# Performance work log

Hardware: AMD Instinct MI355X
Metric: run time of the kernel (lower is better)

Reference implementation:

```python
import jax, jax.numpy as jnp
import numpy as np

NUM_HEADS = 16
EMBED_DIM = 1024
HEAD_DIM = EMBED_DIM // NUM_HEADS  # 64


def setup_inputs() -> dict:
    key = jax.random.key(0)
    k1, k2, k3 = jax.random.split(key, 3)
    x = jax.random.normal(k1, (2, 2048, EMBED_DIM), dtype=jnp.float32)
    # torch Linear(head_dim, 3*head_dim): weight [3*hd, hd], bias [3*hd]
    # stored here as W_qkv [hd, 3*hd] so that y = x @ W_qkv + b
    lim = 1.0 / np.sqrt(HEAD_DIM)
    W_qkv = jax.random.uniform(k2, (HEAD_DIM, 3 * HEAD_DIM), minval=-lim, maxval=lim, dtype=jnp.float32)
    b_qkv = jax.random.uniform(k3, (3 * HEAD_DIM,), minval=-lim, maxval=lim, dtype=jnp.float32)
    return {"x": x, "W_qkv": W_qkv, "b_qkv": b_qkv}


def reference(x, W_qkv, b_qkv):
    B, T, E = x.shape
    # [B, T, E] -> [B, H, T, hd]
    xh = x.reshape(B, T, NUM_HEADS, HEAD_DIM).transpose(0, 2, 1, 3)
    qkv = xh @ W_qkv + b_qkv  # [B, H, T, 3*hd], shared weights across heads
    q, k, v = jnp.split(qkv, 3, axis=-1)
    scale = 1.0 / jnp.sqrt(jnp.asarray(HEAD_DIM, dtype=x.dtype))
    scores = jnp.einsum('bhqd,bhkd->bhqk', q, k) * scale  # [B, H, T, T]
    attn = jax.nn.softmax(scores, axis=-1)
    out = jnp.einsum('bhqk,bhkd->bhqd', attn, v)  # [B, H, T, hd]
    return out.transpose(0, 2, 1, 3).reshape(B, T, E)
```

## Files before the change

### kernel.cpp

```cpp
#include <hip/hip_runtime.h>
#include <hip/hip_bf16.h>

#define T_SEQ   2048
#define EMBED   1024
#define HD      64
#define NHEADS  16
#define NBH     32
#define QSCALE  0.18033688011112042f

typedef __attribute__((ext_vector_type(8))) short short8;
typedef __attribute__((ext_vector_type(4))) float f32x4;
typedef __attribute__((ext_vector_type(2))) unsigned int uint2v;
typedef __attribute__((ext_vector_type(4))) unsigned int uint4v;

#if __has_builtin(__builtin_amdgcn_exp2f)
#define EXP2F __builtin_amdgcn_exp2f
#else
#define EXP2F exp2f
#endif

__device__ __forceinline__ ushort bf16r(float f) {
  union { float f; unsigned u; } v; v.f = f;
  return (ushort)((v.u + 0x8000u) >> 16);
}

__device__ __forceinline__ unsigned pk2bf_perm(float a, float b) {
  union { float f; unsigned u; } ua, ub; ua.f = a; ub.f = b;
  return __builtin_amdgcn_perm(ub.u + 0x8000u, ua.u + 0x8000u, 0x07060302u);
}
#if __has_builtin(__builtin_amdgcn_cvt_pk_bf16_f32)
typedef __attribute__((ext_vector_type(2))) __bf16 bf16x2;
__device__ __forceinline__ unsigned pkbf(float a, float b) {
  union { bf16x2 v; unsigned u; } c;
  c.v = __builtin_amdgcn_cvt_pk_bf16_f32(a, b);
  return c.u;
}
#else
#define pkbf pk2bf_perm
#endif

__device__ __forceinline__ uint2v pl32swap(unsigned a, unsigned b) {
#if __has_builtin(__builtin_amdgcn_permlane32_swap)
  return __builtin_amdgcn_permlane32_swap(a, b, false, false);
#else
  asm("v_permlane32_swap_b32 %0, %1" : "+v"(a), "+v"(b));
  return (uint2v){a, b};
#endif
}
__device__ __forceinline__ uint2v pl16swap(unsigned a, unsigned b) {
#if __has_builtin(__builtin_amdgcn_permlane16_swap)
  return __builtin_amdgcn_permlane16_swap(a, b, false, false);
#else
  asm("v_permlane16_swap_b32 %0, %1" : "+v"(a), "+v"(b));
  return (uint2v){a, b};
#endif
}

__device__ __forceinline__ void async16(const ushort* g, ushort* l) {
  __builtin_amdgcn_global_load_lds(
      (const __attribute__((address_space(1))) unsigned int*)g,
      (__attribute__((address_space(3))) unsigned int*)l, 16, 0, 0);
}

__global__ __launch_bounds__(256) void prep_w(const float* __restrict__ W,
                                              ushort* __restrict__ Wg) {
  const int i = blockIdx.x * 256 + threadIdx.x;
  const int d = i / 192, c = i - d * 192;
  const int phys = c * 64 + (((d >> 3) ^ (c & 7)) << 3) + (d & 7);
  Wg[phys] = bf16r(W[i]);
}

__global__ __launch_bounds__(256) void qkv_proj(
    const float* __restrict__ x, const ushort* __restrict__ Wg,
    const float* __restrict__ bias,
    ushort* __restrict__ Qws, ushort* __restrict__ Kws,
    ushort* __restrict__ Vtws) {
  __shared__ ushort WtL[192 * 64];
  __shared__ float bl[192];

  const int bx = blockIdx.x;
  const int b  = bx >> 9;
  const int h  = (bx >> 5) & 15;
  const int t0 = (bx & 31) * 64;
  const int tid = threadIdx.x;
  const int wave = tid >> 6, lane = tid & 63;
  const int quad = lane >> 4, n16 = lane & 15;

  const int trow = t0 + wave * 16 + n16;
  const float* xr = x + ((size_t)(b * T_SEQ + trow)) * EMBED + h * HD;
  short8 xa[2];
#pragma unroll
  for (int ks = 0; ks < 2; ks++) {
    f32x4 v0 = *(const f32x4*)(xr + ks * 32 + quad * 8);
    f32x4 v1 = *(const f32x4*)(xr + ks * 32 + quad * 8 + 4);
    short8 f;
    ((unsigned*)&f)[0] = pkbf(v0[0], v0[1]);
    ((unsigned*)&f)[1] = pkbf(v0[2], v0[3]);
    ((unsigned*)&f)[2] = pkbf(v1[0], v1[1]);
    ((unsigned*)&f)[3] = pkbf(v1[2], v1[3]);
    xa[ks] = f;
  }

#pragma unroll
  for (int it = 0; it < 6; it++)
    async16(Wg + it * 2048 + tid * 8, WtL + it * 2048 + wave * 512);
  if (tid < 192) bl[tid] = bias[tid];
  __syncthreads();

  const int bh = b * NHEADS + h;
  const size_t qkbase = (size_t)bh * T_SEQ * HD;
  const int tw = t0 + wave * 16;
  const int sw = n16 & 7;

#pragma unroll
  for (int nt = 0; nt < 12; nt++) {
    const ushort* wrow = WtL + (nt * 16 + n16) * 64;
    const short8 wb0 = *(short8*)(wrow + ((quad ^ sw) << 3));
    const short8 wb1 = *(short8*)(wrow + (((4 | quad) ^ sw) << 3));
    const float bv = bl[nt * 16 + n16];
    f32x4 acc = (f32x4){0.f, 0.f, 0.f, 0.f};
    acc = __builtin_amdgcn_mfma_f32_16x16x32_bf16(xa[0], wb0, acc, 0, 0, 0);
    acc = __builtin_amdgcn_mfma_f32_16x16x32_bf16(xa[1], wb1, acc, 0, 0, 0);
    if (nt < 4) {
      const int d = nt * 16 + n16;
#pragma unroll
      for (int r = 0; r < 4; r++)
        Qws[qkbase + (size_t)(tw + quad * 4 + r) * HD + d] =
            bf16r((acc[r] + bv) * QSCALE);
    } else if (nt < 8) {
      const int d = (nt - 4) * 16 + n16;
#pragma unroll
      for (int r = 0; r < 4; r++)
        Kws[qkbase + (size_t)(tw + quad * 4 + r) * HD + d] =
            bf16r(acc[r] + bv);
    } else {
      const int d = (nt - 8) * 16 + n16;
      const int tcol = tw + quad * 4;
      uint2v pk;
      pk.x = pkbf(acc[0] + bv, acc[1] + bv);
      pk.y = pkbf(acc[2] + bv, acc[3] + bv);
      *(uint2v*)(Vtws + (size_t)(bh * HD + d) * T_SEQ + tcol) = pk;
    }
  }
}

__global__ __launch_bounds__(256) void flash_attn(
    const ushort* __restrict__ Qws, const ushort* __restrict__ Kws,
    const ushort* __restrict__ Vtws, float* __restrict__ out) {
  __shared__ ushort Ks[4][64 * 64];
  __shared__ ushort Vs[4][64 * 64];

  const int bx = blockIdx.x;
  const int bh = bx & 31;
  const int q0 = (bx >> 5) * 128;
  const int b = bh >> 4, h = bh & 15;
  const int tid = threadIdx.x;
  const int wave = tid >> 6, lane = tid & 63;
  const int quad = lane >> 4, n16 = lane & 15;

  const ushort* Qb = Qws + (size_t)bh * T_SEQ * HD;
  const ushort* Kb = Kws + (size_t)bh * T_SEQ * HD;
  const ushort* Vb = Vtws + (size_t)bh * HD * T_SEQ;

  short8 qa[2][2];
#pragma unroll
  for (int hf = 0; hf < 2; hf++)
#pragma unroll
    for (int ks = 0; ks < 2; ks++) {
      const int row = q0 + wave * 32 + hf * 16 + n16;
      qa[hf][ks] = *(const short8*)(Qb + (size_t)row * HD + ks * 32 + quad * 8);
    }

  const int sr = tid >> 3, sp = tid & 7;
  const int sl = (sp ^ (sr & 7)) * 8;
  const ushort* srcK0 = Kb + (size_t)sr * HD + sl;
  const ushort* srcK1 = Kb + (size_t)(sr + 32) * HD + sl;
  const ushort* srcV0 = Vb + (size_t)sr * T_SEQ + sl;
  const ushort* srcV1 = Vb + (size_t)(sr + 32) * T_SEQ + sl;

  int foff[2];
#pragma unroll
  for (int ks = 0; ks < 2; ks++)
    foff[ks] = n16 * 64 + ((((ks << 2) | quad) ^ (n16 & 7)) << 3);

  short8 ones;
#pragma unroll
  for (int j = 0; j < 8; j++) ones[j] = (short)0x3F80;

  f32x4 o[2][4];
  f32x4 lA[2];
#pragma unroll
  for (int hf = 0; hf < 2; hf++) {
    lA[hf] = (f32x4){0.f, 0.f, 0.f, 0.f};
#pragma unroll
    for (int nt = 0; nt < 4; nt++) o[hf][nt] = (f32x4){0.f, 0.f, 0.f, 0.f};
  }

  async16(srcK0, Ks[0] + wave * 512);
  async16(srcK1, Ks[0] + 2048 + wave * 512);
  async16(srcV0, Vs[0] + wave * 512);
  async16(srcV1, Vs[0] + 2048 + wave * 512);
  async16(srcK0 + 64 * HD, Ks[1] + wave * 512);
  async16(srcK1 + 64 * HD, Ks[1] + 2048 + wave * 512);
  async16(srcV0 + 64, Vs[1] + wave * 512);
  async16(srcV1 + 64, Vs[1] + 2048 + wave * 512);

  for (int kt = 0; kt < 32; kt++) {
    const int cb = kt & 3;
    if (kt < 30) {
      const int pb = (kt + 2) & 3;
      const size_t kK = (size_t)(kt + 2) * 64 * HD;
      const size_t kV = (size_t)(kt + 2) * 64;
      async16(srcK0 + kK, Ks[pb] + wave * 512);
      async16(srcK1 + kK, Ks[pb] + 2048 + wave * 512);
      async16(srcV0 + kV, Vs[pb] + wave * 512);
      async16(srcV1 + kV, Vs[pb] + 2048 + wave * 512);
    }
    __builtin_amdgcn_sched_barrier(0);
    if (kt < 30)       asm volatile("s_waitcnt vmcnt(8)" ::: "memory");
    else if (kt == 30) asm volatile("s_waitcnt vmcnt(4)" ::: "memory");
    else               asm volatile("s_waitcnt vmcnt(0)" ::: "memory");
    __builtin_amdgcn_s_barrier();
    __builtin_amdgcn_sched_barrier(0);

    const ushort* Kt = Ks[cb];
    const ushort* Vt = Vs[cb];

    f32x4 s0[4], s1[4];
    __builtin_amdgcn_s_setprio(1);
#pragma unroll
    for (int nt = 0; nt < 4; nt++) {
      const short8 ka0 = *(short8*)(Kt + (nt << 10) + foff[0]);
      const short8 ka1 = *(short8*)(Kt + (nt << 10) + foff[1]);
      f32x4 a0 = (f32x4){0.f, 0.f, 0.f, 0.f};
      f32x4 a1 = (f32x4){0.f, 0.f, 0.f, 0.f};
      a0 = __builtin_amdgcn_mfma_f32_16x16x32_bf16(ka0, qa[0][0], a0, 0, 0, 0);
      a0 = __builtin_amdgcn_mfma_f32_16x16x32_bf16(ka1, qa[0][1], a0, 0, 0, 0);
      a1 = __builtin_amdgcn_mfma_f32_16x16x32_bf16(ka0, qa[1][0], a1, 0, 0, 0);
      a1 = __builtin_amdgcn_mfma_f32_16x16x32_bf16(ka1, qa[1][1], a1, 0, 0, 0);
      s0[nt] = a0;
      s1[nt] = a1;
    }
    __builtin_amdgcn_s_setprio(0);

    short8 pa[2][2];
#pragma unroll
    for (int hf = 0; hf < 2; hf++) {
      unsigned P01[4], P23[4];
#pragma unroll
      for (int nt = 0; nt < 4; nt++) {
        const f32x4 sv = hf ? s1[nt] : s0[nt];
        float p0 = EXP2F(sv[0]), p1 = EXP2F(sv[1]);
        float p2 = EXP2F(sv[2]), p3 = EXP2F(sv[3]);
        P01[nt] = pkbf(p0, p1);
        P23[nt] = pkbf(p2, p3);
      }
#pragma unroll
      for (int ks = 0; ks < 2; ks++) {
        uint2v tA = pl32swap(P01[2 * ks], P01[2 * ks + 1]);
        uint2v uA = pl16swap(tA.x, tA.y);
        uint2v tB = pl32swap(P23[2 * ks], P23[2 * ks + 1]);
        uint2v uB = pl16swap(tB.x, tB.y);
        union { uint4v u; short8 s; } c;
        c.u = (uint4v){uA.x, uB.x, uA.y, uB.y};
        pa[hf][ks] = c.s;
      }
    }

    __builtin_amdgcn_s_setprio(1);
#pragma unroll
    for (int nt = 0; nt < 4; nt++) {
      const short8 vb0 = *(short8*)(Vt + (nt << 10) + foff[0]);
      const short8 vb1 = *(short8*)(Vt + (nt << 10) + foff[1]);
      o[0][nt] = __builtin_amdgcn_mfma_f32_16x16x32_bf16(pa[0][0], vb0, o[0][nt], 0, 0, 0);
      o[0][nt] = __builtin_amdgcn_mfma_f32_16x16x32_bf16(pa[0][1], vb1, o[0][nt], 0, 0, 0);
      o[1][nt] = __builtin_amdgcn_mfma_f32_16x16x32_bf16(pa[1][0], vb0, o[1][nt], 0, 0, 0);
      o[1][nt] = __builtin_amdgcn_mfma_f32_16x16x32_bf16(pa[1][1], vb1, o[1][nt], 0, 0, 0);
    }
#pragma unroll
    for (int hf = 0; hf < 2; hf++) {
      lA[hf] = __builtin_amdgcn_mfma_f32_16x16x32_bf16(pa[hf][0], ones, lA[hf], 0, 0, 0);
      lA[hf] = __builtin_amdgcn_mfma_f32_16x16x32_bf16(pa[hf][1], ones, lA[hf], 0, 0, 0);
    }
    __builtin_amdgcn_s_setprio(0);
  }

#pragma unroll
  for (int hf = 0; hf < 2; hf++) {
#pragma unroll
    for (int r = 0; r < 4; r++) {
      const float rl = 1.0f / lA[hf][r];
      const int row = q0 + wave * 32 + hf * 16 + quad * 4 + r;
#pragma unroll
      for (int nt = 0; nt < 4; nt++) {
        const int d = nt * 16 + n16;
        out[(size_t)(b * T_SEQ + row) * EMBED + h * HD + d] = o[hf][nt][r] * rl;
      }
    }
  }
}

extern "C" void kernel_launch(void* const* d_in, const int* in_sizes, int n_in,
                              void* d_out, int out_size, void* d_ws, size_t ws_size,
                              hipStream_t stream) {
  (void)in_sizes; (void)n_in; (void)out_size; (void)ws_size;
  const float* x    = (const float*)d_in[0];
  const float* W    = (const float*)d_in[1];
  const float* bias = (const float*)d_in[2];
  float* out = (float*)d_out;

  const size_t elems = (size_t)NBH * T_SEQ * HD;
  ushort* Qws  = (ushort*)d_ws;
  ushort* Kws  = Qws + elems;
  ushort* Vtws = Kws + elems;
  ushort* Wg   = Vtws + elems;

  prep_w<<<dim3(48), dim3(256), 0, stream>>>(W, Wg);
  qkv_proj<<<dim3(1024), dim3(256), 0, stream>>>(x, Wg, bias, Qws, Kws, Vtws);
  flash_attn<<<dim3(512), dim3(256), 0, stream>>>(Qws, Kws, Vtws, out);
}
```

Before: 123.7 us.

## Process K/V tiles in pairs per barrier and vectorize Q/K projection stores

```diff
diff --git a/kernel.cpp b/kernel.cpp
--- a/kernel.cpp
+++ b/kernel.cpp
@@ -76,7 +76,7 @@
     ushort* __restrict__ Qws, ushort* __restrict__ Kws,
     ushort* __restrict__ Vtws) {
   __shared__ ushort WtL[192 * 64];
-  __shared__ float bl[192];
+  __shared__ __attribute__((aligned(16))) float bl[192];
 
   const int bx = blockIdx.x;
   const int b  = bx >> 9;
@@ -111,29 +111,35 @@
   const size_t qkbase = (size_t)bh * T_SEQ * HD;
   const int tw = t0 + wave * 16;
   const int sw = n16 & 7;
+  const int t = tw + n16;
 
 #pragma unroll
   for (int nt = 0; nt < 12; nt++) {
     const ushort* wrow = WtL + (nt * 16 + n16) * 64;
     const short8 wb0 = *(short8*)(wrow + ((quad ^ sw) << 3));
     const short8 wb1 = *(short8*)(wrow + (((4 | quad) ^ sw) << 3));
-    const float bv = bl[nt * 16 + n16];
-    f32x4 acc = (f32x4){0.f, 0.f, 0.f, 0.f};
-    acc = __builtin_amdgcn_mfma_f32_16x16x32_bf16(xa[0], wb0, acc, 0, 0, 0);
-    acc = __builtin_amdgcn_mfma_f32_16x16x32_bf16(xa[1], wb1, acc, 0, 0, 0);
-    if (nt < 4) {
-      const int d = nt * 16 + n16;
-#pragma unroll
-      for (int r = 0; r < 4; r++)
-        Qws[qkbase + (size_t)(tw + quad * 4 + r) * HD + d] =
-            bf16r((acc[r] + bv) * QSCALE);
-    } else if (nt < 8) {
-      const int d = (nt - 4) * 16 + n16;
-#pragma unroll
-      for (int r = 0; r < 4; r++)
-        Kws[qkbase + (size_t)(tw + quad * 4 + r) * HD + d] =
-            bf16r(acc[r] + bv);
+    if (nt < 8) {
+      f32x4 acc = (f32x4){0.f, 0.f, 0.f, 0.f};
+      acc = __builtin_amdgcn_mfma_f32_16x16x32_bf16(wb0, xa[0], acc, 0, 0, 0);
+      acc = __builtin_amdgcn_mfma_f32_16x16x32_bf16(wb1, xa[1], acc, 0, 0, 0);
+      const f32x4 bv4 = *(const f32x4*)(bl + nt * 16 + quad * 4);
+      uint2v pk;
+      if (nt < 4) {
+        const int d = nt * 16 + quad * 4;
+        pk.x = pkbf((acc[0] + bv4[0]) * QSCALE, (acc[1] + bv4[1]) * QSCALE);
+        pk.y = pkbf((acc[2] + bv4[2]) * QSCALE, (acc[3] + bv4[3]) * QSCALE);
+        *(uint2v*)(Qws + qkbase + (size_t)t * HD + d) = pk;
+      } else {
+        const int d = (nt - 4) * 16 + quad * 4;
+        pk.x = pkbf(acc[0] + bv4[0], acc[1] + bv4[1]);
+        pk.y = pkbf(acc[2] + bv4[2], acc[3] + bv4[3]);
+        *(uint2v*)(Kws + qkbase + (size_t)t * HD + d) = pk;
+      }
     } else {
+      f32x4 acc = (f32x4){0.f, 0.f, 0.f, 0.f};
+      acc = __builtin_amdgcn_mfma_f32_16x16x32_bf16(xa[0], wb0, acc, 0, 0, 0);
+      acc = __builtin_amdgcn_mfma_f32_16x16x32_bf16(xa[1], wb1, acc, 0, 0, 0);
+      const float bv = bl[nt * 16 + n16];
       const int d = (nt - 8) * 16 + n16;
       const int tcol = tw + quad * 4;
       uint2v pk;
@@ -196,36 +202,7 @@
     for (int nt = 0; nt < 4; nt++) o[hf][nt] = (f32x4){0.f, 0.f, 0.f, 0.f};
   }
 
-  async16(srcK0, Ks[0] + wave * 512);
-  async16(srcK1, Ks[0] + 2048 + wave * 512);
-  async16(srcV0, Vs[0] + wave * 512);
-  async16(srcV1, Vs[0] + 2048 + wave * 512);
-  async16(srcK0 + 64 * HD, Ks[1] + wave * 512);
-  async16(srcK1 + 64 * HD, Ks[1] + 2048 + wave * 512);
-  async16(srcV0 + 64, Vs[1] + wave * 512);
-  async16(srcV1 + 64, Vs[1] + 2048 + wave * 512);
-
-  for (int kt = 0; kt < 32; kt++) {
-    const int cb = kt & 3;
-    if (kt < 30) {
-      const int pb = (kt + 2) & 3;
-      const size_t kK = (size_t)(kt + 2) * 64 * HD;
-      const size_t kV = (size_t)(kt + 2) * 64;
-      async16(srcK0 + kK, Ks[pb] + wave * 512);
-      async16(srcK1 + kK, Ks[pb] + 2048 + wave * 512);
-      async16(srcV0 + kV, Vs[pb] + wave * 512);
-      async16(srcV1 + kV, Vs[pb] + 2048 + wave * 512);
-    }
-    __builtin_amdgcn_sched_barrier(0);
-    if (kt < 30)       asm volatile("s_waitcnt vmcnt(8)" ::: "memory");
-    else if (kt == 30) asm volatile("s_waitcnt vmcnt(4)" ::: "memory");
-    else               asm volatile("s_waitcnt vmcnt(0)" ::: "memory");
-    __builtin_amdgcn_s_barrier();
-    __builtin_amdgcn_sched_barrier(0);
-
-    const ushort* Kt = Ks[cb];
-    const ushort* Vt = Vs[cb];
-
+  auto tile = [&](const ushort* Kt, const ushort* Vt) {
     f32x4 s0[4], s1[4];
     __builtin_amdgcn_s_setprio(1);
 #pragma unroll
@@ -283,6 +260,37 @@
       lA[hf] = __builtin_amdgcn_mfma_f32_16x16x32_bf16(pa[hf][1], ones, lA[hf], 0, 0, 0);
     }
     __builtin_amdgcn_s_setprio(0);
+  };
+
+  async16(srcK0, Ks[0] + wave * 512);
+  async16(srcK1, Ks[0] + 2048 + wave * 512);
+  async16(srcV0, Vs[0] + wave * 512);
+  async16(srcV1, Vs[0] + 2048 + wave * 512);
+  async16(srcK0 + 64 * HD, Ks[1] + wave * 512);
+  async16(srcK1 + 64 * HD, Ks[1] + 2048 + wave * 512);
+  async16(srcV0 + 64, Vs[1] + wave * 512);
+  async16(srcV1 + 64, Vs[1] + 2048 + wave * 512);
+  srcK0 += 128 * HD; srcK1 += 128 * HD; srcV0 += 128; srcV1 += 128;
+
+  for (int j = 0; j < 16; j++) {
+    __builtin_amdgcn_sched_barrier(0);
+    asm volatile("s_waitcnt vmcnt(0)" ::: "memory");
+    __builtin_amdgcn_s_barrier();
+    __builtin_amdgcn_sched_barrier(0);
+    const int b0 = (j & 1) << 1;
+    if (j < 15) {
+      async16(srcK0, Ks[b0 ^ 2] + wave * 512);
+      async16(srcK1, Ks[b0 ^ 2] + 2048 + wave * 512);
+      async16(srcV0, Vs[b0 ^ 2] + wave * 512);
+      async16(srcV1, Vs[b0 ^ 2] + 2048 + wave * 512);
+      async16(srcK0 + 64 * HD, Ks[(b0 ^ 2) | 1] + wave * 512);
+      async16(srcK1 + 64 * HD, Ks[(b0 ^ 2) | 1] + 2048 + wave * 512);
+      async16(srcV0 + 64, Vs[(b0 ^ 2) | 1] + wave * 512);
+      async16(srcV1 + 64, Vs[(b0 ^ 2) | 1] + 2048 + wave * 512);
+      srcK0 += 128 * HD; srcK1 += 128 * HD; srcV0 += 128; srcV1 += 128;
+    }
+    tile(Ks[b0], Vs[b0]);
+    tile(Ks[b0 | 1], Vs[b0 | 1]);
   }
 
 #pragma unroll
```

Result: slower. 128.7 us (+4.0%).
